# Performance work log

Hardware: AMD Instinct MI355X
Metric: run time of the kernel (lower is better)

Reference implementation:

```python
import jax, jax.numpy as jnp
import numpy as np

B, C, T, V, D, H, KT = 64, 3, 256, 21, 128, 4, 9


def _adjacency():
    rng = np.random.default_rng(0)
    Araw = (rng.random((V, V)) < 0.3).astype(np.float32)
    Araw = np.maximum(Araw, Araw.T)
    np.fill_diagonal(Araw, 1.0)
    deg = Araw.sum(1)
    Anorm = Araw / np.sqrt(deg[:, None] * deg[None, :])  # D^-1/2 A D^-1/2
    return Araw.astype(np.float32), Anorm.astype(np.float32)


def setup_inputs() -> dict:
    key = jax.random.key(0)
    ks = jax.random.split(key, 24)
    g = lambda i, shape, sc=0.05: jax.random.normal(ks[i], shape, dtype=jnp.float32) * sc
    Araw, Anorm = _adjacency()
    return {
        'x': jax.random.normal(ks[0], (B, C, T, V), dtype=jnp.float32),
        'coord_w': g(1, (C, D)), 'coord_b': g(2, (D,)),
        'joint_emb': g(3, (V, D)),
        'graph_bias': jnp.asarray(Araw),  # nn.Parameter(A.clone().float())
        'wq': g(4, (D, D)), 'bq': g(5, (D,)),
        'wk': g(6, (D, D)), 'bk': g(7, (D,)),
        'wv': g(8, (D, D)), 'bv': g(9, (D,)),
        'wo': g(10, (D, D)), 'bo': g(11, (D,)),
        'gcn_w1': g(12, (D, D)), 'gcn_b1': g(13, (D,)),
        'tcn_w1': g(14, (D, D, KT, 1)), 'tcn_b1': g(15, (D,)),
        'gcn_w2': g(16, (D, D)), 'gcn_b2': g(17, (D,)),
        'tcn_w2': g(18, (D, D, KT, 1)), 'tcn_b2': g(19, (D,)),
        'A': jnp.asarray(Anorm),  # fixed normalized adjacency buffer
    }


def _stgcn(x, A, gw, gb, tw, tb):
    # x: [B, D, T, V]; spatial graph conv then temporal conv, residual.
    res = x
    y = jnp.einsum('bctv,vw->bctw', x, A)              # neighbor aggregation
    y = jnp.einsum('bctv,dc->bdtv', y, gw) + gb[None, :, None, None]
    y = jax.nn.relu(y)
    y = jax.lax.conv_general_dilated(
        y, tw, window_strides=(1, 1), padding=((KT // 2, KT // 2), (0, 0)),
        dimension_numbers=('NCHW', 'OIHW', 'NCHW'))     # temporal conv, kernel 9
    y = y + tb[None, :, None, None]
    return jax.nn.relu(y + res)


def reference(x, coord_w, coord_b, joint_emb, graph_bias, wq, bq, wk, bk, wv, bv,
              wo, bo, gcn_w1, gcn_b1, tcn_w1, tcn_b1, gcn_w2, gcn_b2, tcn_w2,
              tcn_b2, A):
    b, c, t, v = x.shape
    d = coord_w.shape[1]
    dh = d // H
    scale = jnp.float32(1.0 / np.sqrt(dh))
    coords = x.transpose(0, 2, 3, 1).reshape(b * t, v, c)      # [N, V, 3]
    feat = coords @ coord_w + coord_b + joint_emb              # LearnedJointEncoding
    q = (feat @ wq + bq).reshape(-1, v, H, dh)
    k = (feat @ wk + bk).reshape(-1, v, H, dh)
    val = (feat @ wv + bv).reshape(-1, v, H, dh)
    scores = jnp.einsum('nihd,njhd->nhij', q, k) * scale + graph_bias[None, None]
    attn = jax.nn.softmax(scores, axis=-1)                     # [N, H, V, V]
    out = jnp.einsum('nhij,njhd->nihd', attn, val).reshape(-1, v, d)
    feat = out @ wo + bo
    feat = feat.reshape(b, t, v, d).transpose(0, 3, 1, 2)       # [B, D, T, V]
    feat = _stgcn(feat, A, gcn_w1, gcn_b1, tcn_w1, tcn_b1)
    feat = _stgcn(feat, A, gcn_w2, gcn_b2, tcn_w2, tcn_b2)
    return feat, attn
```

## Files before the change

### kernel.cpp

```cpp
#include <hip/hip_runtime.h>
#include <hip/hip_bf16.h>

typedef __hip_bfloat16 bf16;
typedef __attribute__((ext_vector_type(8))) short short8v;
typedef __attribute__((ext_vector_type(4))) float float4v;

#define BB   64
#define CC   3
#define TLEN 256
#define VJ   21
#define DM   128
#define NH   4
#define DH   32
#define KT   9
#define NFR  (BB*TLEN)
#define MTOK (NFR*VJ)
#define NIN  22

__device__ __forceinline__ float b2f(bf16 x){ return __bfloat162float(x); }
__device__ __forceinline__ bf16  f2b(float x){ return __float2bfloat16(x); }
__device__ __forceinline__ float hb2f(short s){ return __uint_as_float(((unsigned)(unsigned short)s) << 16); }
__device__ __forceinline__ float lo16(unsigned u){ return __uint_as_float(u << 16); }
__device__ __forceinline__ float hi16(unsigned u){ return __uint_as_float(u & 0xffff0000u); }

__global__ void detect_dtype(const void* __restrict__ xin, int nus, int* __restrict__ flag){
  const unsigned short* u = (const unsigned short*)xin;
  int lim = nus < 65536 ? nus : 65536;
  int bad = 0;
  for (int k = threadIdx.x; k < lim; k += 256){
    float f = __uint_as_float(((unsigned)u[k]) << 16);
    if (!(fabsf(f) < 1e6f)) bad = 1;
  }
  if (bad) atomicOr(flag, 1);
}

struct ConvArgs { const void* src[NIN]; int off[NIN+1]; };

__global__ void convert_inputs(ConvArgs a, bf16* __restrict__ dst,
                               const int* __restrict__ flag, int total){
  int i = blockIdx.x*256 + threadIdx.x;
  if (i >= total) return;
  bool isf32 = (*flag != 0);
  int k = 0;
  while (i >= a.off[k+1]) ++k;
  int j = i - a.off[k];
  float v;
  if (isf32) v = ((const float*)a.src[k])[j];
  else       v = __uint_as_float(((unsigned)((const unsigned short*)a.src[k])[j]) << 16);
  dst[i] = f2b(v);
}

__global__ void prep_weights(const bf16* __restrict__ wq, const bf16* __restrict__ wk,
                             const bf16* __restrict__ wv, const bf16* __restrict__ wo,
                             const bf16* __restrict__ tw1, const bf16* __restrict__ tw2,
                             bf16* __restrict__ wqT, bf16* __restrict__ wkT,
                             bf16* __restrict__ wvT, bf16* __restrict__ woT,
                             bf16* __restrict__ twT1, bf16* __restrict__ twT2){
  int i = blockIdx.x*256 + threadIdx.x;
  if (i < DM*DM){
    int d = i >> 7, e = i & 127;
    wqT[i] = wq[e*DM + d];
    wkT[i] = wk[e*DM + d];
    wvT[i] = wv[e*DM + d];
    woT[i] = wo[e*DM + d];
  }
  if (i < KT*DM*DM){
    int c = i & 127; int d = (i >> 7) & 127; int tap = i >> 14;
    twT1[i] = tw1[(d*DM + c)*KT + tap];
    twT2[i] = tw2[(d*DM + c)*KT + tap];
  }
}

__global__ __launch_bounds__(512) void qkv_gemm(const bf16* __restrict__ x,
                                                const bf16* __restrict__ cw,
                                                const bf16* __restrict__ cb,
                                                const bf16* __restrict__ je,
                                                const bf16* __restrict__ BtQ,
                                                const bf16* __restrict__ BtK,
                                                const bf16* __restrict__ BtV,
                                                const bf16* __restrict__ bq,
                                                const bf16* __restrict__ bk,
                                                const bf16* __restrict__ bv,
                                                bf16* __restrict__ Oq,
                                                bf16* __restrict__ Ok,
                                                bf16* __restrict__ Ov){
  __shared__ short8v lds[128*16];
  __shared__ float sxf[128][4];
  const int tid = threadIdx.x;
  const int r0  = blockIdx.x*128;
  {
    int tok = tid >> 2, c = tid & 3;
    if (tok < 128 && c < 3){
      int n = r0 + tok;
      int v = n % VJ; int t = (n / VJ) % TLEN; int b = n / (VJ*TLEN);
      sxf[tok][c] = b2f(x[((size_t)(b*CC + c)*TLEN + t)*VJ + v]);
    }
  }
  __syncthreads();
  for (int i = tid; i < 128*16; i += 512){
    int row = i >> 4, c0 = i & 15;
    int n = r0 + row; int v = n % VJ;
    short8v cw0 = *reinterpret_cast<const short8v*>(cw + 0*DM + c0*8);
    short8v cw1 = *reinterpret_cast<const short8v*>(cw + 1*DM + c0*8);
    short8v cw2 = *reinterpret_cast<const short8v*>(cw + 2*DM + c0*8);
    short8v cbv = *reinterpret_cast<const short8v*>(cb + c0*8);
    short8v jev = *reinterpret_cast<const short8v*>(je + v*DM + c0*8);
    float x0 = sxf[row][0], x1 = sxf[row][1], x2 = sxf[row][2];
    short8v out;
    #pragma unroll
    for (int e = 0; e < 8; ++e){
      float f = hb2f(cbv[e]) + hb2f(jev[e]);
      f = fmaf(x0, hb2f(cw0[e]), f);
      f = fmaf(x1, hb2f(cw1[e]), f);
      f = fmaf(x2, hb2f(cw2[e]), f);
      bf16 h = f2b(f);
      out[e] = *reinterpret_cast<short*>(&h);
    }
    lds[row*16 + (c0 ^ (row & 7))] = out;
  }
  __syncthreads();
  const int lane = tid & 63;
  const int wid  = tid >> 6;
  const int rbase = (wid >> 2) * 64;
  const int nt0   = (wid & 3) * 2;
  const int l15 = lane & 15, l4 = lane >> 4;
  #pragma unroll
  for (int w = 0; w < 3; ++w){
    const bf16* Bt  = (w==0) ? BtQ : (w==1) ? BtK : BtV;
    const bf16* bia = (w==0) ? bq  : (w==1) ? bk  : bv;
    bf16*       Out = (w==0) ? Oq  : (w==1) ? Ok  : Ov;
    short8v breg[2][4];
    #pragma unroll
    for (int ntl = 0; ntl < 2; ++ntl)
      #pragma unroll
      for (int ks = 0; ks < 4; ++ks)
        breg[ntl][ks] = *reinterpret_cast<const short8v*>(Bt + ((nt0+ntl)*16 + l15)*DM + ks*32 + l4*8);
    float4v acc[4][2];
    #pragma unroll
    for (int rt = 0; rt < 4; ++rt){ acc[rt][0] = (float4v){0,0,0,0}; acc[rt][1] = (float4v){0,0,0,0}; }
    #pragma unroll
    for (int rt = 0; rt < 4; ++rt){
      const int ldsRow = rbase + rt*16 + l15;
      #pragma unroll
      for (int ks = 0; ks < 4; ++ks){
        short8v a = lds[ldsRow*16 + ((ks*4 + l4) ^ (ldsRow & 7))];
        acc[rt][0] = __builtin_amdgcn_mfma_f32_16x16x32_bf16(a, breg[0][ks], acc[rt][0], 0,0,0);
        acc[rt][1] = __builtin_amdgcn_mfma_f32_16x16x32_bf16(a, breg[1][ks], acc[rt][1], 0,0,0);
      }
    }
    #pragma unroll
    for (int rt = 0; rt < 4; ++rt)
      #pragma unroll
      for (int ntl = 0; ntl < 2; ++ntl){
        int col = (nt0+ntl)*16 + l15;
        float bvv = b2f(bia[col]);
        #pragma unroll
        for (int j = 0; j < 4; ++j)
          Out[(size_t)(r0 + rbase + rt*16 + l4*4 + j)*DM + col] = f2b(acc[rt][ntl][j] + bvv);
      }
  }
}

template<int NTAPS, bool RELU, bool RESID>
__global__ __launch_bounds__(512, 4) void conv_gemm(const bf16* __restrict__ A,
                                                    const bf16* __restrict__ Bt,
                                                    const bf16* __restrict__ bias,
                                                    const bf16* resid,
                                                    bf16* Cout){
  constexpr int HALO = (NTAPS/2)*VJ;
  constexpr int ROWS = 128 + 2*HALO;
  __shared__ short8v lds[ROWS*16];
  const int tid = threadIdx.x;
  const int r0  = blockIdx.x*128;
  for (int i = tid; i < ROWS*16; i += 512){
    int row = i >> 4, c0 = i & 15;
    long tok = (long)r0 - HALO + row;
    if (tok < 0) tok = 0;
    if (tok > MTOK-1) tok = MTOK-1;
    lds[row*16 + (c0 ^ (row & 7))] = *reinterpret_cast<const short8v*>(A + tok*DM + c0*8);
  }
  __syncthreads();
  const int lane = tid & 63;
  const int wid  = tid >> 6;
  const int rbase = (wid >> 2) * 64;
  const int nt0   = (wid & 3) * 2;
  const int l15 = lane & 15, l4 = lane >> 4;
  int trow[4];
  #pragma unroll
  for (int rt = 0; rt < 4; ++rt)
    trow[rt] = ((r0 + rbase + rt*16 + l15) / VJ) % TLEN;
  float4v acc[4][2];
  #pragma unroll
  for (int rt = 0; rt < 4; ++rt){ acc[rt][0] = (float4v){0,0,0,0}; acc[rt][1] = (float4v){0,0,0,0}; }

  const bf16* bptr = Bt + (nt0*16 + l15)*DM + l4*8;
  short8v bcur[2][4], bnxt[2][4];
  #pragma unroll
  for (int ntl = 0; ntl < 2; ++ntl)
    #pragma unroll
    for (int ks = 0; ks < 4; ++ks)
      bcur[ntl][ks] = *reinterpret_cast<const short8v*>(bptr + ntl*16*DM + ks*32);

  #pragma unroll
  for (int tap = 0; tap < NTAPS; ++tap){
    if (tap + 1 < NTAPS){
      const bf16* bp = bptr + (size_t)(tap+1)*DM*DM;
      #pragma unroll
      for (int ntl = 0; ntl < 2; ++ntl)
        #pragma unroll
        for (int ks = 0; ks < 4; ++ks)
          bnxt[ntl][ks] = *reinterpret_cast<const short8v*>(bp + ntl*16*DM + ks*32);
    }
    const int dt = tap - NTAPS/2;
    #pragma unroll
    for (int rt = 0; rt < 4; ++rt){
      bool valid = true;
      if (NTAPS > 1){
        int ts = trow[rt] + dt;
        valid = (ts >= 0) && (ts < TLEN);
      }
      const int ldsRow = rbase + rt*16 + l15 + HALO + dt*VJ;
      #pragma unroll
      for (int ks = 0; ks < 4; ++ks){
        short8v a = lds[ldsRow*16 + ((ks*4 + l4) ^ (ldsRow & 7))];
        if (NTAPS > 1 && !valid) a = (short8v){0,0,0,0,0,0,0,0};
        acc[rt][0] = __builtin_amdgcn_mfma_f32_16x16x32_bf16(a, bcur[0][ks], acc[rt][0], 0,0,0);
        acc[rt][1] = __builtin_amdgcn_mfma_f32_16x16x32_bf16(a, bcur[1][ks], acc[rt][1], 0,0,0);
      }
    }
    if (tap + 1 < NTAPS){
      #pragma unroll
      for (int ntl = 0; ntl < 2; ++ntl)
        #pragma unroll
        for (int ks = 0; ks < 4; ++ks)
          bcur[ntl][ks] = bnxt[ntl][ks];
    }
  }
  #pragma unroll
  for (int rt = 0; rt < 4; ++rt){
    #pragma unroll
    for (int ntl = 0; ntl < 2; ++ntl){
      int col = (nt0+ntl)*16 + l15;
      float bv = b2f(bias[col]);
      #pragma unroll
      for (int j = 0; j < 4; ++j){
        size_t idx = (size_t)(r0 + rbase + rt*16 + l4*4 + j)*DM + col;
        float val = acc[rt][ntl][j] + bv;
        if (RESID) val += b2f(resid[idx]);
        if (RELU) val = fmaxf(val, 0.f);
        Cout[idx] = f2b(val);
      }
    }
  }
}

__global__ __launch_bounds__(256) void attn_core(const bf16* __restrict__ Q,
                                                 const bf16* __restrict__ K,
                                                 const bf16* __restrict__ V,
                                                 const bf16* __restrict__ gbias,
                                                 const bf16* __restrict__ woT,
                                                 const bf16* __restrict__ bo,
                                                 float* __restrict__ attn_out,
                                                 bf16* __restrict__ feat_out){
  const int n = blockIdx.x;
  const int tid = threadIdx.x;
  __shared__ bf16 skv[3][VJ][136];
  __shared__ float sc[NH*VJ*VJ];
  __shared__ float rmax[NH*VJ], rinv[NH*VJ];
  __shared__ bf16 sgb[VJ*VJ];
  __shared__ short8v sao[32*16];

  for (int i = tid; i < VJ*VJ; i += 256) sgb[i] = gbias[i];
  for (int i = tid; i < 3*VJ*16; i += 256){
    int c0 = i & 15; int v = (i >> 4) % VJ; int w = i / (16*VJ);
    const bf16* src = (w==0 ? Q : (w==1 ? K : V)) + ((size_t)n*VJ + v)*DM + c0*8;
    *reinterpret_cast<short8v*>(&skv[w][v][c0*8]) = *reinterpret_cast<const short8v*>(src);
  }
  __syncthreads();
  const float scale = 0.17677669529663687f;
  for (int idx = tid; idx < NH*VJ*VJ; idx += 256){
    int j = idx % VJ, i2 = (idx/VJ) % VJ, h = idx/(VJ*VJ);
    const unsigned* qr = reinterpret_cast<const unsigned*>(&skv[0][i2][h*DH]);
    const unsigned* kr = reinterpret_cast<const unsigned*>(&skv[1][j][h*DH]);
    float a = 0.f;
    #pragma unroll
    for (int p = 0; p < DH/2; ++p){
      unsigned qa = qr[p], ka = kr[p];
      a = fmaf(lo16(qa), lo16(ka), a);
      a = fmaf(hi16(qa), hi16(ka), a);
    }
    sc[idx] = a*scale + b2f(sgb[i2*VJ + j]);
  }
  __syncthreads();
  for (int r = tid; r < NH*VJ; r += 256){
    float m = -1e30f;
    for (int j = 0; j < VJ; ++j) m = fmaxf(m, sc[r*VJ + j]);
    float s = 0.f;
    for (int j = 0; j < VJ; ++j) s += __expf(sc[r*VJ + j] - m);
    rmax[r] = m; rinv[r] = 1.0f/s;
  }
  __syncthreads();
  for (int idx = tid; idx < NH*VJ*VJ; idx += 256){
    int r = idx / VJ;
    float e = __expf(sc[idx] - rmax[r]) * rinv[r];
    sc[idx] = e;
    attn_out[(size_t)n*(NH*VJ*VJ) + idx] = e;
  }
  __syncthreads();
  for (int i = tid; i < VJ*(DM/2); i += 256){
    int q2 = i & 63; int v = i >> 6;
    int d0 = q2*2; int h = d0 >> 5;
    const float* pr = &sc[(h*VJ + v)*VJ];
    float a0 = 0.f, a1 = 0.f;
    #pragma unroll
    for (int j = 0; j < VJ; ++j){
      unsigned va = *reinterpret_cast<const unsigned*>(&skv[2][j][d0]);
      float p = pr[j];
      a0 = fmaf(p, lo16(va), a0);
      a1 = fmaf(p, hi16(va), a1);
    }
    bf16 b0 = f2b(a0), b1 = f2b(a1);
    unsigned u0 = *reinterpret_cast<unsigned short*>(&b0);
    unsigned u1 = *reinterpret_cast<unsigned short*>(&b1);
    unsigned* lp = reinterpret_cast<unsigned*>(&sao[v*16 + ((q2 >> 2) ^ (v & 7))]);
    lp[q2 & 3] = u0 | (u1 << 16);
  }
  __syncthreads();
  const int lane = tid & 63;
  const int wid  = tid >> 6;
  const int l15 = lane & 15, l4 = lane >> 4;
  float4v acc[2][2];
  #pragma unroll
  for (int mt = 0; mt < 2; ++mt){ acc[mt][0] = (float4v){0,0,0,0}; acc[mt][1] = (float4v){0,0,0,0}; }
  #pragma unroll
  for (int ks = 0; ks < 4; ++ks){
    short8v bfr[2];
    #pragma unroll
    for (int ct = 0; ct < 2; ++ct)
      bfr[ct] = *reinterpret_cast<const short8v*>(woT + (wid*32 + ct*16 + l15)*DM + ks*32 + l4*8);
    #pragma unroll
    for (int mt = 0; mt < 2; ++mt){
      int row = mt*16 + l15;
      short8v a = sao[row*16 + ((ks*4 + l4) ^ (row & 7))];
      acc[mt][0] = __builtin_amdgcn_mfma_f32_16x16x32_bf16(a, bfr[0], acc[mt][0], 0,0,0);
      acc[mt][1] = __builtin_amdgcn_mfma_f32_16x16x32_bf16(a, bfr[1], acc[mt][1], 0,0,0);
    }
  }
  #pragma unroll
  for (int mt = 0; mt < 2; ++mt){
    #pragma unroll
    for (int ct = 0; ct < 2; ++ct){
      int col = wid*32 + ct*16 + l15;
      float bov = b2f(bo[col]);
      #pragma unroll
      for (int j = 0; j < 4; ++j){
        int row = mt*16 + l4*4 + j;
        if (row < VJ)
          feat_out[((size_t)n*VJ + row)*DM + col] = f2b(acc[mt][ct][j] + bov);
      }
    }
  }
}

__global__ __launch_bounds__(256) void agg_kernel(const bf16* __restrict__ fin,
                                                  const bf16* __restrict__ An,
                                                  bf16* __restrict__ aout){
  const int n = blockIdx.x;
  const int tid = threadIdx.x;
  __shared__ bf16 sx[VJ][136];
  __shared__ float sA[VJ*VJ];
  for (int i = tid; i < VJ*VJ; i += 256) sA[i] = b2f(An[i]);
  for (int i = tid; i < VJ*16; i += 256){
    int c0 = i & 15, v = i >> 4;
    *reinterpret_cast<short8v*>(&sx[v][c0*8]) =
      *reinterpret_cast<const short8v*>(fin + ((size_t)n*VJ + v)*DM + c0*8);
  }
  __syncthreads();
  for (int i = tid; i < VJ*16; i += 256){
    int c0 = i & 15, w = i >> 4;
    float acc[8] = {0,0,0,0,0,0,0,0};
    #pragma unroll
    for (int u = 0; u < VJ; ++u){
      float a = sA[u*VJ + w];
      short8v xv = *reinterpret_cast<const short8v*>(&sx[u][c0*8]);
      #pragma unroll
      for (int e = 0; e < 8; ++e) acc[e] = fmaf(a, hb2f(xv[e]), acc[e]);
    }
    short8v out;
    #pragma unroll
    for (int e = 0; e < 8; ++e){ bf16 h = f2b(acc[e]); out[e] = *reinterpret_cast<short*>(&h); }
    *reinterpret_cast<short8v*>(aout + ((size_t)n*VJ + w)*DM + c0*8) = out;
  }
}

__global__ __launch_bounds__(256) void transpose_out(const bf16* __restrict__ fin,
                                                     float* __restrict__ fout){
  const int bid = blockIdx.x;
  const int b   = bid >> 5;
  const int rem = bid & 31;
  const int t0  = (rem >> 2) * 32;
  const int d0  = (rem & 3) * 32;
  __shared__ bf16 tile[32][VJ][33];
  const int tid = threadIdx.x;
  for (int idx = tid; idx < 32*VJ*32; idx += 256){
    int dl = idx & 31;
    int v  = (idx >> 5) % VJ;
    int tl = idx / (32*VJ);
    tile[tl][v][dl] = fin[((size_t)(b*TLEN + t0 + tl)*VJ + v)*DM + d0 + dl];
  }
  __syncthreads();
  for (int idx = tid; idx < 32*VJ*32; idx += 256){
    int j  = idx % (32*VJ);
    int dl = idx / (32*VJ);
    int tl = j / VJ, v = j % VJ;
    fout[((size_t)(b*DM + d0 + dl)*TLEN + t0 + tl)*VJ + v] = b2f(tile[tl][v][dl]);
  }
}

extern "C" void kernel_launch(void* const* d_in, const int* in_sizes, int n_in,
                              void* d_out, int out_size, void* d_ws, size_t ws_size,
                              hipStream_t stream){
  const size_t featElems = (size_t)MTOK*DM;
  float* outf    = (float*)d_out;
  float* attnOut = outf + featElems;
  bf16* qbuf = (bf16*)d_out;
  bf16* kbuf = qbuf + featElems;

  char* wp = (char*)d_ws;
  auto alloc = [&](size_t bytes)->char*{ char* p = wp; wp += (bytes + 15) & ~(size_t)15; return p; };
  int*  flag = (int*)alloc(16);
  ConvArgs ca; int total = 0;
  for (int i = 0; i < NIN; ++i){ ca.src[i] = d_in[i]; ca.off[i] = total; total += in_sizes[i]; }
  ca.off[NIN] = total;
  bf16* cin   = (bf16*)alloc((size_t)total*2);
  bf16* wqT   = (bf16*)alloc(DM*DM*2);
  bf16* wkT   = (bf16*)alloc(DM*DM*2);
  bf16* wvT   = (bf16*)alloc(DM*DM*2);
  bf16* woT   = (bf16*)alloc(DM*DM*2);
  bf16* twT1  = (bf16*)alloc(KT*DM*DM*2);
  bf16* twT2  = (bf16*)alloc(KT*DM*DM*2);
  bf16* featA = (bf16*)alloc(featElems*2);
  bf16* bufV  = (bf16*)alloc(featElems*2);
  if ((size_t)(wp - (char*)d_ws) > ws_size) return;

  const bf16* x    = cin + ca.off[0];
  const bf16* cw   = cin + ca.off[1];
  const bf16* cb   = cin + ca.off[2];
  const bf16* je   = cin + ca.off[3];
  const bf16* gbias= cin + ca.off[4];
  const bf16* wq   = cin + ca.off[5];
  const bf16* bq   = cin + ca.off[6];
  const bf16* wk   = cin + ca.off[7];
  const bf16* bk   = cin + ca.off[8];
  const bf16* wv   = cin + ca.off[9];
  const bf16* bv   = cin + ca.off[10];
  const bf16* wo   = cin + ca.off[11];
  const bf16* bo   = cin + ca.off[12];
  const bf16* gw1  = cin + ca.off[13];
  const bf16* gb1  = cin + ca.off[14];
  const bf16* tw1  = cin + ca.off[15];
  const bf16* tb1  = cin + ca.off[16];
  const bf16* gw2  = cin + ca.off[17];
  const bf16* gb2  = cin + ca.off[18];
  const bf16* tw2  = cin + ca.off[19];
  const bf16* tb2  = cin + ca.off[20];
  const bf16* An   = cin + ca.off[21];

  const int GB = MTOK/128;
  hipMemsetAsync(flag, 0, sizeof(int), stream);
  detect_dtype<<<1, 256, 0, stream>>>(d_in[0], in_sizes[0], flag);
  convert_inputs<<<(total + 255)/256, 256, 0, stream>>>(ca, cin, flag, total);
  prep_weights<<<(KT*DM*DM + 255)/256, 256, 0, stream>>>(wq, wk, wv, wo, tw1, tw2,
                                                         wqT, wkT, wvT, woT, twT1, twT2);
  qkv_gemm<<<GB, 512, 0, stream>>>(x, cw, cb, je, wqT, wkT, wvT, bq, bk, bv,
                                   qbuf, kbuf, bufV);
  attn_core<<<NFR, 256, 0, stream>>>(qbuf, kbuf, bufV, gbias, woT, bo, attnOut, featA);
  agg_kernel<<<NFR, 256, 0, stream>>>(featA, An, qbuf);
  conv_gemm<1,true,false><<<GB, 512, 0, stream>>>(qbuf, gw1, gb1, nullptr, kbuf);
  conv_gemm<9,true,true><<<GB, 512, 0, stream>>>(kbuf, twT1, tb1, featA, featA);
  agg_kernel<<<NFR, 256, 0, stream>>>(featA, An, qbuf);
  conv_gemm<1,true,false><<<GB, 512, 0, stream>>>(qbuf, gw2, gb2, nullptr, kbuf);
  conv_gemm<9,true,true><<<GB, 512, 0, stream>>>(kbuf, twT2, tb2, featA, featA);
  transpose_out<<<BB*(TLEN/32)*(DM/32), 256, 0, stream>>>(featA, outf);
}
```

Before: 1.306 ms.

## Reorder token layout to (b,v,t) so temporal conv tiles avoid large halos

```diff
diff --git a/kernel.cpp b/kernel.cpp
--- a/kernel.cpp
+++ b/kernel.cpp
@@ -16,6 +16,7 @@
 #define NFR  (BB*TLEN)
 #define MTOK (NFR*VJ)
 #define NIN  22
+
 
 __device__ __forceinline__ float b2f(bf16 x){ return __bfloat162float(x); }
 __device__ __forceinline__ bf16  f2b(float x){ return __float2bfloat16(x); }
@@ -88,23 +89,22 @@
   __shared__ float sxf[128][4];
   const int tid = threadIdx.x;
   const int r0  = blockIdx.x*128;
+  const int bvi = r0 >> 8;
+  const int t0  = r0 & (TLEN-1);
+  const int blk_b = bvi / VJ, blk_v = bvi % VJ;
   {
     int tok = tid >> 2, c = tid & 3;
-    if (tok < 128 && c < 3){
-      int n = r0 + tok;
-      int v = n % VJ; int t = (n / VJ) % TLEN; int b = n / (VJ*TLEN);
-      sxf[tok][c] = b2f(x[((size_t)(b*CC + c)*TLEN + t)*VJ + v]);
-    }
+    if (tok < 128 && c < 3)
+      sxf[tok][c] = b2f(x[((size_t)(blk_b*CC + c)*TLEN + t0 + tok)*VJ + blk_v]);
   }
   __syncthreads();
   for (int i = tid; i < 128*16; i += 512){
     int row = i >> 4, c0 = i & 15;
-    int n = r0 + row; int v = n % VJ;
     short8v cw0 = *reinterpret_cast<const short8v*>(cw + 0*DM + c0*8);
     short8v cw1 = *reinterpret_cast<const short8v*>(cw + 1*DM + c0*8);
     short8v cw2 = *reinterpret_cast<const short8v*>(cw + 2*DM + c0*8);
     short8v cbv = *reinterpret_cast<const short8v*>(cb + c0*8);
-    short8v jev = *reinterpret_cast<const short8v*>(je + v*DM + c0*8);
+    short8v jev = *reinterpret_cast<const short8v*>(je + blk_v*DM + c0*8);
     float x0 = sxf[row][0], x1 = sxf[row][1], x2 = sxf[row][2];
     short8v out;
     #pragma unroll
@@ -167,17 +167,19 @@
                                                     const bf16* __restrict__ bias,
                                                     const bf16* resid,
                                                     bf16* Cout){
-  constexpr int HALO = (NTAPS/2)*VJ;
-  constexpr int ROWS = 128 + 2*HALO;
+  constexpr int HT   = NTAPS/2;
+  constexpr int ROWS = 128 + 2*HT;
   __shared__ short8v lds[ROWS*16];
   const int tid = threadIdx.x;
   const int r0  = blockIdx.x*128;
+  const int t0  = r0 & (TLEN-1);
+  const long mb = r0 - t0;
   for (int i = tid; i < ROWS*16; i += 512){
     int row = i >> 4, c0 = i & 15;
-    long tok = (long)r0 - HALO + row;
-    if (tok < 0) tok = 0;
-    if (tok > MTOK-1) tok = MTOK-1;
-    lds[row*16 + (c0 ^ (row & 7))] = *reinterpret_cast<const short8v*>(A + tok*DM + c0*8);
+    int t = t0 + row - HT;
+    if (t < 0) t = 0;
+    if (t > TLEN-1) t = TLEN-1;
+    lds[row*16 + (c0 ^ (row & 7))] = *reinterpret_cast<const short8v*>(A + (mb + t)*DM + c0*8);
   }
   __syncthreads();
   const int lane = tid & 63;
@@ -185,55 +187,36 @@
   const int rbase = (wid >> 2) * 64;
   const int nt0   = (wid & 3) * 2;
   const int l15 = lane & 15, l4 = lane >> 4;
-  int trow[4];
-  #pragma unroll
-  for (int rt = 0; rt < 4; ++rt)
-    trow[rt] = ((r0 + rbase + rt*16 + l15) / VJ) % TLEN;
   float4v acc[4][2];
   #pragma unroll
   for (int rt = 0; rt < 4; ++rt){ acc[rt][0] = (float4v){0,0,0,0}; acc[rt][1] = (float4v){0,0,0,0}; }
 
-  const bf16* bptr = Bt + (nt0*16 + l15)*DM + l4*8;
-  short8v bcur[2][4], bnxt[2][4];
-  #pragma unroll
-  for (int ntl = 0; ntl < 2; ++ntl)
-    #pragma unroll
-    for (int ks = 0; ks < 4; ++ks)
-      bcur[ntl][ks] = *reinterpret_cast<const short8v*>(bptr + ntl*16*DM + ks*32);
-
   #pragma unroll
   for (int tap = 0; tap < NTAPS; ++tap){
-    if (tap + 1 < NTAPS){
-      const bf16* bp = bptr + (size_t)(tap+1)*DM*DM;
-      #pragma unroll
-      for (int ntl = 0; ntl < 2; ++ntl)
-        #pragma unroll
-        for (int ks = 0; ks < 4; ++ks)
-          bnxt[ntl][ks] = *reinterpret_cast<const short8v*>(bp + ntl*16*DM + ks*32);
-    }
-    const int dt = tap - NTAPS/2;
+    const bf16* Btap = Bt + (size_t)tap*DM*DM;
+    short8v breg[2][4];
+    #pragma unroll
+    for (int ntl = 0; ntl < 2; ++ntl)
+      #pragma unroll
+      for (int ks = 0; ks < 4; ++ks)
+        breg[ntl][ks] = *reinterpret_cast<const short8v*>(Btap + ((nt0+ntl)*16 + l15)*DM + ks*32 + l4*8);
+    const int dt = tap - HT;
     #pragma unroll
     for (int rt = 0; rt < 4; ++rt){
+      const int tl = rbase + rt*16 + l15;
       bool valid = true;
       if (NTAPS > 1){
-        int ts = trow[rt] + dt;
+        int ts = t0 + tl + dt;
         valid = (ts >= 0) && (ts < TLEN);
       }
-      const int ldsRow = rbase + rt*16 + l15 + HALO + dt*VJ;
+      const int ldsRow = tl + HT + dt;
       #pragma unroll
       for (int ks = 0; ks < 4; ++ks){
         short8v a = lds[ldsRow*16 + ((ks*4 + l4) ^ (ldsRow & 7))];
         if (NTAPS > 1 && !valid) a = (short8v){0,0,0,0,0,0,0,0};
-        acc[rt][0] = __builtin_amdgcn_mfma_f32_16x16x32_bf16(a, bcur[0][ks], acc[rt][0], 0,0,0);
-        acc[rt][1] = __builtin_amdgcn_mfma_f32_16x16x32_bf16(a, bcur[1][ks], acc[rt][1], 0,0,0);
-      }
-    }
-    if (tap + 1 < NTAPS){
-      #pragma unroll
-      for (int ntl = 0; ntl < 2; ++ntl)
-        #pragma unroll
-        for (int ks = 0; ks < 4; ++ks)
-          bcur[ntl][ks] = bnxt[ntl][ks];
+        acc[rt][0] = __builtin_amdgcn_mfma_f32_16x16x32_bf16(a, breg[0][ks], acc[rt][0], 0,0,0);
+        acc[rt][1] = __builtin_amdgcn_mfma_f32_16x16x32_bf16(a, breg[1][ks], acc[rt][1], 0,0,0);
+      }
     }
   }
   #pragma unroll
@@ -263,6 +246,7 @@
                                                  float* __restrict__ attn_out,
                                                  bf16* __restrict__ feat_out){
   const int n = blockIdx.x;
+  const int bb = n / TLEN, t = n % TLEN;
   const int tid = threadIdx.x;
   __shared__ bf16 skv[3][VJ][136];
   __shared__ float sc[NH*VJ*VJ];
@@ -273,7 +257,8 @@
   for (int i = tid; i < VJ*VJ; i += 256) sgb[i] = gbias[i];
   for (int i = tid; i < 3*VJ*16; i += 256){
     int c0 = i & 15; int v = (i >> 4) % VJ; int w = i / (16*VJ);
-    const bf16* src = (w==0 ? Q : (w==1 ? K : V)) + ((size_t)n*VJ + v)*DM + c0*8;
+    size_t m = ((size_t)bb*VJ + v)*TLEN + t;
+    const bf16* src = (w==0 ? Q : (w==1 ? K : V)) + m*DM + c0*8;
     *reinterpret_cast<short8v*>(&skv[w][v][c0*8]) = *reinterpret_cast<const short8v*>(src);
   }
   __syncthreads();
@@ -356,7 +341,7 @@
       for (int j = 0; j < 4; ++j){
         int row = mt*16 + l4*4 + j;
         if (row < VJ)
-          feat_out[((size_t)n*VJ + row)*DM + col] = f2b(acc[mt][ct][j] + bov);
+          feat_out[(((size_t)bb*VJ + row)*TLEN + t)*DM + col] = f2b(acc[mt][ct][j] + bov);
       }
     }
   }
@@ -366,14 +351,16 @@
                                                   const bf16* __restrict__ An,
                                                   bf16* __restrict__ aout){
   const int n = blockIdx.x;
+  const int bb = n / TLEN, t = n % TLEN;
   const int tid = threadIdx.x;
   __shared__ bf16 sx[VJ][136];
   __shared__ float sA[VJ*VJ];
   for (int i = tid; i < VJ*VJ; i += 256) sA[i] = b2f(An[i]);
   for (int i = tid; i < VJ*16; i += 256){
     int c0 = i & 15, v = i >> 4;
+    size_t m = ((size_t)bb*VJ + v)*TLEN + t;
     *reinterpret_cast<short8v*>(&sx[v][c0*8]) =
-      *reinterpret_cast<const short8v*>(fin + ((size_t)n*VJ + v)*DM + c0*8);
+      *reinterpret_cast<const short8v*>(fin + m*DM + c0*8);
   }
   __syncthreads();
   for (int i = tid; i < VJ*16; i += 256){
@@ -389,7 +376,8 @@
     short8v out;
     #pragma unroll
     for (int e = 0; e < 8; ++e){ bf16 h = f2b(acc[e]); out[e] = *reinterpret_cast<short*>(&h); }
-    *reinterpret_cast<short8v*>(aout + ((size_t)n*VJ + w)*DM + c0*8) = out;
+    size_t m = ((size_t)bb*VJ + w)*TLEN + t;
+    *reinterpret_cast<short8v*>(aout + m*DM + c0*8) = out;
   }
 }
 
@@ -406,7 +394,7 @@
     int dl = idx & 31;
     int v  = (idx >> 5) % VJ;
     int tl = idx / (32*VJ);
-    tile[tl][v][dl] = fin[((size_t)(b*TLEN + t0 + tl)*VJ + v)*DM + d0 + dl];
+    tile[tl][v][dl] = fin[(((size_t)b*VJ + v)*TLEN + t0 + tl)*DM + d0 + dl];
   }
   __syncthreads();
   for (int idx = tid; idx < 32*VJ*32; idx += 256){
```

Measured after the change: 1.271 ms. 2.6% less time.
